# Optimization experiments

Hardware: AMD Instinct MI355X
Metric: run time of the kernel (lower is better)

The kernel has to match this reference:

```python
import jax, jax.numpy as jnp
import numpy as np

B, T, D, NH, FF, L, NCLS, CELL = 4, 64, 128, 4, 512, 2, 7, 64
DIMS = (600, 342, 300)


def layernorm(x, g, b, eps=1e-5):
    m = jnp.mean(x, -1, keepdims=True)
    v = jnp.mean((x - m) ** 2, -1, keepdims=True)
    return (x - m) / jnp.sqrt(v + eps) * g + b


def mha(x, Wqkv, bqkv, Wo, bo):
    N, S, Dm = x.shape
    hd = Dm // NH
    q, k, v = jnp.split(x @ Wqkv + bqkv, 3, axis=-1)
    q = q.reshape(N, S, NH, hd).transpose(0, 2, 1, 3) / jnp.float32(hd) ** 0.5
    k = k.reshape(N, S, NH, hd).transpose(0, 2, 1, 3)
    v = v.reshape(N, S, NH, hd).transpose(0, 2, 1, 3)
    att = jax.nn.softmax(jnp.einsum('nhqd,nhkd->nhqk', q, k), axis=-1)
    o = jnp.einsum('nhqk,nhkd->nhqd', att, v).transpose(0, 2, 1, 3).reshape(N, S, Dm)
    return o @ Wo + bo


def _l2norm(x):
    return x / jnp.maximum(jnp.linalg.norm(x, axis=-1, keepdims=True), 1e-12)


def _model(x_text, x_vis, x_aud, Wp_text, bp_text, Wp_vis, bp_vis, Wp_aud, bp_aud,
           lang1, lang2, Wl1, bl1, Wl2, bl2, phase_text, phase_vis, phase_aud,
           t_Wqkv, t_bqkv, t_Wo, t_bo, t_g1, t_b1, t_W1, t_bf1, t_W2, t_bf2, t_g2, t_b2,
           meas_r, meas_i, fc_W1, fc_b1, fc_W2, fc_b2):
    b, t = x_text.shape[0], x_text.shape[1]
    # modality projections + ReLU
    reps = [jax.nn.relu(x @ W + bb) for x, W, bb in
            ((x_text, Wp_text, bp_text), (x_vis, Wp_vis, bp_vis), (x_aud, Wp_aud, bp_aud))]
    l1 = jnp.broadcast_to(lang1, (b, t, lang1.shape[-1]))
    l2 = jnp.broadcast_to(lang2, (b, t, lang2.shape[-1]))
    lrep1 = jax.nn.relu(l1 @ Wl1 + bl1)
    lrep2 = jax.nn.relu(l2 @ Wl2 + bl2)
    amps = [_l2norm(r) for r in reps]
    lamp1, lamp2 = _l2norm(lrep1), _l2norm(lrep2)
    # phase embedding: smask is all-ones so index is always 0 -> single learned phase vector
    phases = [jnp.broadcast_to(p, (b, t, D)) for p in (phase_text, phase_vis, phase_aud)]
    cmul = lambda ph, a: (a * jnp.cos(ph), a * jnp.sin(ph))
    pure = [cmul(ph, a) for ph, a in zip(phases, amps)]
    ls1 = cmul(phases[0], lamp1)
    ls2 = cmul(phases[0], lamp2)
    # Hadamard gate analog on (real, imag)
    s2 = jnp.float32(2.0) ** -0.5
    h1 = ((ls1[0] + ls1[1]) * s2, (ls1[0] - ls1[1]) * s2)
    h2 = ((ls2[0] + ls2[1]) * s2, (ls2[0] - ls2[1]) * s2)
    # CNOT-style entanglement: complex elementwise product, renormalized to a pure state
    er = h1[0] * h2[0] - h1[1] * h2[1]
    ei = h1[0] * h2[1] + h1[1] * h2[0]
    en = jnp.maximum(jnp.sqrt(jnp.sum(er * er + ei * ei, -1, keepdims=True)), 1e-12)
    ent = (er / en, ei / en)

    def outer(st):  # rho = v v^dagger, v = r + i*im
        r, i = st
        rr = jnp.einsum('btd,bte->btde', r, r) + jnp.einsum('btd,bte->btde', i, i)
        ri = jnp.einsum('btd,bte->btde', i, r) - jnp.einsum('btd,bte->btde', r, i)
        return rr, ri

    mats = [outer(s) for s in pure] + [outer(ent)]
    w = jnp.concatenate([jnp.linalg.norm(r, axis=-1, keepdims=True)
                         for r in reps + [lrep1]], -1)
    w = jax.nn.softmax(w, -1)  # [B,T,4]
    rho_r = sum(w[..., m:m + 1, None] * mats[m][0] for m in range(4))
    rho_i = sum(w[..., m:m + 1, None] * mats[m][1] for m in range(4))
    # seq blocks: same block applied independently per timestep to real and imag parts
    # -> vectorize the Python loop over T (and the real/imag pair) into one batch dim
    x = jnp.concatenate([rho_r, rho_i], 0).reshape(2 * b * t, D, D)
    for l in range(L):
        x = layernorm(x + mha(x, t_Wqkv[l], t_bqkv[l], t_Wo[l], t_bo[l]), t_g1[l], t_b1[l])
        x = layernorm(x + (jax.nn.relu(x @ t_W1[l] + t_bf1[l]) @ t_W2[l] + t_bf2[l]),
                      t_g2[l], t_b2[l])
    x = x.reshape(2, b, t, D, D)
    rho_r, rho_i = x[0], x[1]
    # quantum measurement: p_k = Re(v_k^dagger rho v_k), v_k normalized complex vectors
    mn = jnp.maximum(jnp.sqrt(jnp.sum(meas_r ** 2 + meas_i ** 2, -1, keepdims=True)), 1e-12)
    vr, vi = meas_r / mn, meas_i / mn  # [K=D, D]
    ar = jnp.einsum('btde,ke->btkd', rho_r, vr) - jnp.einsum('btde,ke->btkd', rho_i, vi)
    ai = jnp.einsum('btde,ke->btkd', rho_r, vi) + jnp.einsum('btde,ke->btkd', rho_i, vr)
    probs = jnp.einsum('kd,btkd->btk', vr, ar) + jnp.einsum('kd,btkd->btk', vi, ai)
    logits = jax.nn.relu(probs @ fc_W1 + fc_b1) @ fc_W2 + fc_b2
    return jax.nn.log_softmax(logits, -1)  # [B,T,NCLS]


def setup_inputs():
    key = jax.random.key(0)
    ks = iter(jax.random.split(key, 32))
    rn = lambda shape, s=0.05: jax.random.normal(next(ks), shape, dtype=jnp.float32) * s
    z = lambda shape: jnp.zeros(shape, jnp.float32)
    o = lambda shape: jnp.ones(shape, jnp.float32)
    return dict(
        x_text=rn((B, T, DIMS[0]), 1.0), x_vis=rn((B, T, DIMS[1]), 1.0), x_aud=rn((B, T, DIMS[2]), 1.0),
        Wp_text=rn((DIMS[0], D)), bp_text=z((D,)),
        Wp_vis=rn((DIMS[1], D)), bp_vis=z((D,)),
        Wp_aud=rn((DIMS[2], D)), bp_aud=z((D,)),
        lang1=rn((1, 1, DIMS[2]), 1.0), lang2=rn((1, 1, DIMS[2]), 1.0),
        Wl1=rn((DIMS[2], D)), bl1=z((D,)), Wl2=rn((DIMS[2], D)), bl2=z((D,)),
        phase_text=rn((D,), 1.0), phase_vis=rn((D,), 1.0), phase_aud=rn((D,), 1.0),
        t_Wqkv=rn((L, D, 3 * D)), t_bqkv=z((L, 3 * D)),
        t_Wo=rn((L, D, D)), t_bo=z((L, D)),
        t_g1=o((L, D)), t_b1=z((L, D)),
        t_W1=rn((L, D, FF)), t_bf1=z((L, FF)),
        t_W2=rn((L, FF, D)), t_bf2=z((L, D)),
        t_g2=o((L, D)), t_b2=z((L, D)),
        meas_r=rn((D, D), 1.0), meas_i=rn((D, D), 1.0),
        fc_W1=rn((D, CELL)), fc_b1=z((CELL,)), fc_W2=rn((CELL, NCLS)), fc_b2=z((NCLS,)),
    )


def reference(x_text, x_vis, x_aud, Wp_text, bp_text, Wp_vis, bp_vis, Wp_aud, bp_aud,
              lang1, lang2, Wl1, bl1, Wl2, bl2, phase_text, phase_vis, phase_aud,
              t_Wqkv, t_bqkv, t_Wo, t_bo, t_g1, t_b1, t_W1, t_bf1, t_W2, t_bf2, t_g2, t_b2,
              meas_r, meas_i, fc_W1, fc_b1, fc_W2, fc_b2):
    return _model(x_text, x_vis, x_aud, Wp_text, bp_text, Wp_vis, bp_vis, Wp_aud, bp_aud,
                  lang1, lang2, Wl1, bl1, Wl2, bl2, phase_text, phase_vis, phase_aud,
                  t_Wqkv, t_bqkv, t_Wo, t_bo, t_g1, t_b1, t_W1, t_bf1, t_W2, t_bf2, t_g2, t_b2,
                  meas_r, meas_i, fc_W1, fc_b1, fc_W2, fc_b2)
```

## Files before the change

kernel.cpp:

```cpp
#include <hip/hip_runtime.h>
#include <hip/hip_bf16.h>

typedef __hip_bfloat16 bf16;
typedef short short8 __attribute__((ext_vector_type(8)));
typedef float f32x4 __attribute__((ext_vector_type(4)));
typedef unsigned uint2v __attribute__((ext_vector_type(2)));

__device__ __forceinline__ float b2f(bf16 v){ return __bfloat162float(v); }

__device__ __forceinline__ short f2bs(float f){
  union { __hip_bfloat16 b; short s; } u; u.b = __float2bfloat16(f); return u.s;
}
__device__ __forceinline__ float bs2f(short s){
  union { short s; __hip_bfloat16 b; } u; u.s = s; return __bfloat162float(u.b);
}
__device__ __forceinline__ unsigned pk2(float a, float b){
  return ((unsigned)(unsigned short)f2bs(a)) | (((unsigned)(unsigned short)f2bs(b)) << 16);
}

__device__ __forceinline__ float wred_sum(float v){
  #pragma unroll
  for (int o = 32; o > 0; o >>= 1) v += __shfl_xor(v, o, 64);
  return v;
}

__device__ __forceinline__ void gload_lds16(const void* g, void* l){
  __builtin_amdgcn_global_load_lds((const __attribute__((address_space(1))) unsigned*)g,
                                   (__attribute__((address_space(3))) unsigned*)l, 16, 0, 0);
}

__device__ __forceinline__ unsigned swzA(unsigned a){ return a ^ (((a >> 8) & 7u) << 4); }
__device__ __forceinline__ unsigned swzB(unsigned a){ return a ^ (((a >> 7) & 3u) << 4); }

template<int DIMN>
__device__ void modality(const float* x, const float* W, const float* bia, const float* ph,
                         float* PURE, float* RNORM, int m, int bt, float* xs, float* red)
{
  int tid = threadIdx.x;
  for (int i = tid; i < DIMN; i += 128) xs[i] = x[bt*DIMN + i];
  __syncthreads();
  float a0 = 0.f, a1 = 0.f, a2 = 0.f, a3 = 0.f;
  int k = 0;
  for (; k + 4 <= DIMN; k += 4){
    a0 = fmaf(xs[k],   W[(k  )*128 + tid], a0);
    a1 = fmaf(xs[k+1], W[(k+1)*128 + tid], a1);
    a2 = fmaf(xs[k+2], W[(k+2)*128 + tid], a2);
    a3 = fmaf(xs[k+3], W[(k+3)*128 + tid], a3);
  }
  for (; k < DIMN; k++) a0 = fmaf(xs[k], W[k*128 + tid], a0);
  float acc = bia[tid] + ((a0 + a1) + (a2 + a3));
  float rep = fmaxf(acc, 0.f);
  float s = wred_sum(rep*rep);
  int wid = tid >> 6, lane = tid & 63;
  if (lane == 0) red[wid] = s;
  __syncthreads();
  float nrm = sqrtf(red[0] + red[1]);
  float amp = rep / fmaxf(nrm, 1e-12f);
  float p = ph[tid];
  PURE[bt*768 + m*128 + tid]       = amp * cosf(p);
  PURE[bt*768 + (3+m)*128 + tid]   = amp * sinf(p);
  if (tid == 0) RNORM[bt*4 + m] = nrm;
}

__global__ void prep_kernel(
    const float* __restrict__ Wqkv, const float* __restrict__ Wo,
    const float* __restrict__ W1, const float* __restrict__ W2,
    short* __restrict__ WqkvT, short* __restrict__ WoT,
    short* __restrict__ W1T, short* __restrict__ W2T,
    const float* xt, const float* xv, const float* xa,
    const float* Wpt, const float* bpt, const float* Wpv, const float* bpv,
    const float* Wpa, const float* bpa,
    const float* pht, const float* phv, const float* pha,
    float* PURE, float* RNORM,
    const float* l1, const float* l2,
    const float* Wl1, const float* bl1, const float* Wl2, const float* bl2,
    float* LANGB,
    const float* mr, const float* mi, float* VMEAS, short* VMEASB)
{
  __shared__ float xs[600];
  __shared__ float xs2a[300];
  __shared__ float red[4];
  __shared__ float tile[32][33];
  int b = blockIdx.x, tid = threadIdx.x;

  if (b < 384){
    int l = b / 192, bb = b - l*192;
    const float* in; short* out; int K, N, kt, nt_;
    bool isW2 = false;
    if (bb < 48)      { in = Wqkv; out = WqkvT; K = 128; N = 384; kt = bb & 3;  nt_ = bb >> 2; }
    else if (bb < 64) { int t = bb-48;  in = Wo; out = WoT; K = 128; N = 128; kt = t & 3;  nt_ = t >> 2; }
    else if (bb < 128){ int t = bb-64;  in = W1; out = W1T; K = 128; N = 512; kt = t & 3;  nt_ = t >> 2; }
    else              { int t = bb-128; in = W2; out = W2T; K = 512; N = 128; kt = t & 15; nt_ = t >> 4; isW2 = true; }
    int base = l * K * N;
    int kk0 = kt*32, nn0 = nt_*32;
    int r0 = tid >> 5, c = tid & 31;
    #pragma unroll
    for (int i = 0; i < 8; i++){
      int r = i*4 + r0;
      tile[r][c] = in[base + (kk0 + r)*N + nn0 + c];
    }
    __syncthreads();
    #pragma unroll
    for (int i = 0; i < 8; i++){
      int rr = i*4 + r0;
      float v = tile[c][rr];
      int oi;
      if (!isW2) oi = (nn0 + rr)*K + kk0 + c;
      else       oi = kt*4096 + (nn0 + rr)*32 + c;
      out[base + oi] = f2bs(v);
    }
    return;
  }
  if (b < 1152){
    int idx = b - 384;
    int bt = idx & 255, m = idx >> 8;
    if (m == 0)      modality<600>(xt, Wpt, bpt, pht, PURE, RNORM, 0, bt, xs, red);
    else if (m == 1) modality<342>(xv, Wpv, bpv, phv, PURE, RNORM, 1, bt, xs, red);
    else             modality<300>(xa, Wpa, bpa, pha, PURE, RNORM, 2, bt, xs, red);
    return;
  }
  if (b >= 1153){
    int k = b - 1153;
    float a = mr[k*128 + tid], bb2 = mi[k*128 + tid];
    float ws = wred_sum(a*a + bb2*bb2);
    int wid = tid >> 6, lane = tid & 63;
    if (lane == 0) red[wid] = ws;
    __syncthreads();
    float inv = 1.f / fmaxf(sqrtf(red[0] + red[1]), 1e-12f);
    float vr = a * inv, vi = bb2 * inv;
    int i = k*128 + tid;
    VMEAS[i]          = vr;
    VMEAS[16384 + i]  = vi;
    VMEASB[i]         = f2bs(vr);
    VMEASB[16384 + i] = f2bs(vi);
    VMEASB[32768 + i] = f2bs(-vi);
    return;
  }
  for (int i = tid; i < 300; i += 128){ xs[i] = l1[i]; xs2a[i] = l2[i]; }
  __syncthreads();
  float p10=0,p11=0,p12=0,p13=0, p20=0,p21=0,p22=0,p23=0;
  for (int k = 0; k < 300; k += 4){
    p10 = fmaf(xs[k],    Wl1[(k  )*128+tid], p10);
    p11 = fmaf(xs[k+1],  Wl1[(k+1)*128+tid], p11);
    p12 = fmaf(xs[k+2],  Wl1[(k+2)*128+tid], p12);
    p13 = fmaf(xs[k+3],  Wl1[(k+3)*128+tid], p13);
    p20 = fmaf(xs2a[k],  Wl2[(k  )*128+tid], p20);
    p21 = fmaf(xs2a[k+1],Wl2[(k+1)*128+tid], p21);
    p22 = fmaf(xs2a[k+2],Wl2[(k+2)*128+tid], p22);
    p23 = fmaf(xs2a[k+3],Wl2[(k+3)*128+tid], p23);
  }
  float a1 = bl1[tid] + ((p10+p11)+(p12+p13));
  float a2 = bl2[tid] + ((p20+p21)+(p22+p23));
  a1 = fmaxf(a1, 0.f); a2 = fmaxf(a2, 0.f);
  int wid = tid >> 6, lane = tid & 63;
  float s1 = wred_sum(a1*a1), s2 = wred_sum(a2*a2);
  if (lane == 0){ red[wid] = s1; red[2+wid] = s2; }
  __syncthreads();
  float n1 = sqrtf(red[0] + red[1]);
  float n2 = sqrtf(red[2] + red[3]);
  float lamp1 = a1 / fmaxf(n1, 1e-12f);
  float lamp2 = a2 / fmaxf(n2, 1e-12f);
  float ph = pht[tid];
  float c = cosf(ph), s = sinf(ph);
  const float s2c = 0.70710678118654752f;
  float h1r = (lamp1*c + lamp1*s)*s2c, h1i = (lamp1*c - lamp1*s)*s2c;
  float h2r = (lamp2*c + lamp2*s)*s2c, h2i = (lamp2*c - lamp2*s)*s2c;
  float er = h1r*h2r - h1i*h2i;
  float ei = h1r*h2i + h1i*h2r;
  __syncthreads();
  float se = wred_sum(er*er + ei*ei);
  if (lane == 0) red[wid] = se;
  __syncthreads();
  float en = fmaxf(sqrtf(red[0] + red[1]), 1e-12f);
  LANGB[tid]       = er / en;
  LANGB[128 + tid] = ei / en;
  if (tid == 0) LANGB[256] = n1;
}

__global__ __launch_bounds__(256) void rho_kernel(const float* PURE, const float* RNORM,
                                                  const float* LANGB, short* Xb)
{
  __shared__ float rv[4][128], iv[4][128], wsm[4];
  int bt = blockIdx.x & 255, half = blockIdx.x >> 8;
  int tid = threadIdx.x;
  for (int i = tid; i < 1024; i += 256){
    int d = i & 127;
    if (i < 768){ int m = i >> 7; float v = PURE[bt*768 + i];
                  if (m < 3) rv[m][d] = v; else iv[m-3][d] = v; }
    else if (i < 896) rv[3][d] = LANGB[d];
    else              iv[3][d] = LANGB[128 + d];
  }
  if (tid == 0){
    float n0 = RNORM[bt*4+0], n1 = RNORM[bt*4+1], n2 = RNORM[bt*4+2], n3 = LANGB[256];
    float mx = fmaxf(fmaxf(n0, n1), fmaxf(n2, n3));
    float e0 = __expf(n0-mx), e1 = __expf(n1-mx), e2 = __expf(n2-mx), e3 = __expf(n3-mx);
    float inv = 1.f / (e0+e1+e2+e3);
    wsm[0]=e0*inv; wsm[1]=e1*inv; wsm[2]=e2*inv; wsm[3]=e3*inv;
  }
  __syncthreads();
  float w0 = wsm[0], w1 = wsm[1], w2 = wsm[2], w3 = wsm[3];
  int lo = half*8192, hi = lo + 8192;
  for (int idx = lo + tid; idx < hi; idx += 256){
    int d = idx >> 7, e = idx & 127;
    float rr = 0.f, ri = 0.f;
    {
      float rd=rv[0][d], re=rv[0][e], id=iv[0][d], ie=iv[0][e];
      rr = fmaf(w0, rd*re + id*ie, rr); ri = fmaf(w0, id*re - rd*ie, ri);
    }{
      float rd=rv[1][d], re=rv[1][e], id=iv[1][d], ie=iv[1][e];
      rr = fmaf(w1, rd*re + id*ie, rr); ri = fmaf(w1, id*re - rd*ie, ri);
    }{
      float rd=rv[2][d], re=rv[2][e], id=iv[2][d], ie=iv[2][e];
      rr = fmaf(w2, rd*re + id*ie, rr); ri = fmaf(w2, id*re - rd*ie, ri);
    }{
      float rd=rv[3][d], re=rv[3][e], id=iv[3][d], ie=iv[3][e];
      rr = fmaf(w3, rd*re + id*ie, rr); ri = fmaf(w3, id*re - rd*ie, ri);
    }
    Xb[(size_t)bt*16384 + idx]        = f2bs(rr);
    Xb[(size_t)(256+bt)*16384 + idx]  = f2bs(ri);
  }
}

__global__ __launch_bounds__(256) void attn_kernel(const short* __restrict__ Xb,
    const short* __restrict__ WqkvT, const float* __restrict__ bqkv,
    bf16* __restrict__ ATTO)
{
  __shared__ __align__(16) char lds_raw[43520];
  short* Vt = (short*)(lds_raw);
  short* Qs = (short*)(lds_raw + 8704);
  short* Ks = (short*)(lds_raw + 18944);
  short* Ps = (short*)(lds_raw + 8704);

  const int n = blockIdx.x, h = blockIdx.y;
  const int tid = threadIdx.x;
  const int wid = tid >> 6, lane = tid & 63;
  const int l15 = lane & 15, quad = lane >> 4;
  const int wb = __builtin_amdgcn_readfirstlane(wid);
  const short* xn = Xb + (size_t)n*16384;
  const char* Wbase = (const char*)WqkvT;

  short8 afr[2][4];
  #pragma unroll
  for (int mi = 0; mi < 2; mi++)
    #pragma unroll
    for (int ks = 0; ks < 4; ks++){
      int row = (wid*2 + mi)*16 + l15;
      afr[mi][ks] = *(const short8*)(xn + row*128 + ks*32 + quad*8);
    }
  #pragma unroll
  for (int j = 0; j < 6; j++){
    int seg = wb*6 + j;
    int slab = seg >> 3;
    unsigned off = (unsigned)((seg & 7)*1024);
    unsigned gbase = (unsigned)((slab*128 + h*32)*256);
    gload_lds16(Wbase + gbase + swzA(off + (unsigned)(lane*16)),
                lds_raw + seg*1024);
  }
  __syncthreads();

  f32x4 acc[2][6];
  #pragma unroll
  for (int mi = 0; mi < 2; mi++)
    #pragma unroll
    for (int nt = 0; nt < 6; nt++){
      f32x4 z = {0.f, 0.f, 0.f, 0.f}; acc[mi][nt] = z;
    }

  #pragma unroll
  for (int ks = 0; ks < 4; ks++){
    #pragma unroll
    for (int nt = 0; nt < 6; nt++){
      int slab = nt >> 1;
      int col = (nt & 1)*16 + l15;
      unsigned a = (unsigned)(col*256 + ks*64 + quad*16);
      short8 bfr = *(const short8*)(lds_raw + slab*8192 + swzA(a));
      #pragma unroll
      for (int mi = 0; mi < 2; mi++)
        acc[mi][nt] = __builtin_amdgcn_mfma_f32_16x16x32_bf16(afr[mi][ks], bfr, acc[mi][nt], 0, 0, 0);
    }
  }
  __syncthreads();

  #pragma unroll
  for (int nt = 0; nt < 6; nt++){
    int sec = nt >> 1;
    int cl = (nt & 1)*16 + l15;
    float bias = bqkv[sec*128 + h*32 + cl];
    #pragma unroll
    for (int mi = 0; mi < 2; mi++){
      int rowb = (wid*2 + mi)*16 + quad*4;
      #pragma unroll
      for (int r = 0; r < 4; r++){
        float v = acc[mi][nt][r] + bias;
        int row = rowb + r;
        if (sec == 0)      Qs[row*40 + cl] = f2bs(v * 0.17677669529663687f);
        else if (sec == 1) Ks[row*40 + cl] = f2bs(v);
        else               Vt[cl*136 + row] = f2bs(v);
      }
    }
  }
  __syncthreads();

  f32x4 s2[8][2];
  {
    short8 qf[2];
    #pragma unroll
    for (int qt = 0; qt < 2; qt++){
      int row = (wid*2 + qt)*16 + l15;
      qf[qt] = *(const short8*)(Qs + row*40 + quad*8);
    }
    #pragma unroll
    for (int kt = 0; kt < 8; kt++){
      int kr = kt*16 + l15;
      short8 kf = *(const short8*)(Ks + kr*40 + quad*8);
      #pragma unroll
      for (int qt = 0; qt < 2; qt++){
        f32x4 z = {0.f, 0.f, 0.f, 0.f};
        s2[kt][qt] = __builtin_amdgcn_mfma_f32_16x16x32_bf16(kf, qf[qt], z, 0, 0, 0);
      }
    }
  }

  #pragma unroll
  for (int qt = 0; qt < 2; qt++){
    float mx = -1e30f;
    #pragma unroll
    for (int kt = 0; kt < 8; kt++)
      #pragma unroll
      for (int r = 0; r < 4; r++) mx = fmaxf(mx, s2[kt][qt][r]);
    mx = fmaxf(mx, __shfl_xor(mx, 16, 64));
    mx = fmaxf(mx, __shfl_xor(mx, 32, 64));
    float sum = 0.f;
    #pragma unroll
    for (int kt = 0; kt < 8; kt++)
      #pragma unroll
      for (int r = 0; r < 4; r++){
        float p = __expf(s2[kt][qt][r] - mx);
        s2[kt][qt][r] = p; sum += p;
      }
    sum += __shfl_xor(sum, 16, 64);
    sum += __shfl_xor(sum, 32, 64);
    float inv = 1.f / sum;
    #pragma unroll
    for (int kt = 0; kt < 8; kt++)
      #pragma unroll
      for (int r = 0; r < 4; r++) s2[kt][qt][r] *= inv;
  }
  __syncthreads();

  #pragma unroll
  for (int kt = 0; kt < 8; kt++){
    #pragma unroll
    for (int qt = 0; qt < 2; qt++){
      int q  = (wid*2 + qt)*16 + l15;
      int k0 = kt*16 + quad*4;
      uint2v v;
      v.x = pk2(s2[kt][qt][0], s2[kt][qt][1]);
      v.y = pk2(s2[kt][qt][2], s2[kt][qt][3]);
      *(uint2v*)((char*)Ps + (unsigned)(q*272 + k0*2)) = v;
    }
  }
  __syncthreads();

  f32x4 o_[2][2];
  #pragma unroll
  for (int mi = 0; mi < 2; mi++)
    #pragma unroll
    for (int n2 = 0; n2 < 2; n2++){
      f32x4 z = {0.f, 0.f, 0.f, 0.f}; o_[mi][n2] = z;
    }
  #pragma unroll
  for (int ks = 0; ks < 4; ks++){
    short8 pf[2];
    #pragma unroll
    for (int mi = 0; mi < 2; mi++){
      int row = (wid*2 + mi)*16 + l15;
      pf[mi] = *(const short8*)(Ps + row*136 + ks*32 + quad*8);
    }
    #pragma unroll
    for (int n2 = 0; n2 < 2; n2++){
      short8 vf = *(const short8*)(Vt + (n2*16 + l15)*136 + ks*32 + quad*8);
      #pragma unroll
      for (int mi = 0; mi < 2; mi++)
        o_[mi][n2] = __builtin_amdgcn_mfma_f32_16x16x32_bf16(pf[mi], vf, o_[mi][n2], 0, 0, 0);
    }
  }
  bf16* on = ATTO + (size_t)n*16384;
  #pragma unroll
  for (int mi = 0; mi < 2; mi++){
    int rowb = (wid*2 + mi)*16 + quad*4;
    #pragma unroll
    for (int n2 = 0; n2 < 2; n2++){
      int col = h*32 + n2*16 + l15;
      #pragma unroll
      for (int r = 0; r < 4; r++)
        on[(rowb + r)*128 + col] = __float2bfloat16(o_[mi][n2][r]);
    }
  }
}

__global__ __launch_bounds__(256, 2) void proj_ffn_kernel(const bf16* __restrict__ SRC,
    short* __restrict__ Xb, const short* __restrict__ WoT,
    const float* __restrict__ bo, const float* __restrict__ g1v,
    const float* __restrict__ bb1,
    const short* __restrict__ W1T, const float* __restrict__ bf1,
    const short* __restrict__ W2C, const float* __restrict__ bf2,
    const float* __restrict__ g2v, const float* __restrict__ bb2)
{
  __shared__ __align__(16) char lds_raw[65536];
  __shared__ float bf1L[512];
  const int n = blockIdx.x, tid = threadIdx.x;
  const int wid = tid >> 6, lane = tid & 63;
  const int l15 = lane & 15, quad = lane >> 4;
  const int wb = __builtin_amdgcn_readfirstlane(wid);
  const short* an = (const short*)SRC + (size_t)n*16384;
  short* xn = Xb + (size_t)n*16384;
  char* XsB = lds_raw + 32768;
  short* Hs = (short*)(lds_raw + 32768);

  short8 af[2][4];
  #pragma unroll
  for (int mi = 0; mi < 2; mi++)
    #pragma unroll
    for (int ks = 0; ks < 4; ks++){
      int row = wid*32 + mi*16 + l15;
      af[mi][ks] = *(const short8*)(an + row*128 + ks*32 + quad*8);
    }
  #pragma unroll
  for (int j = 0; j < 8; j++){
    unsigned L = (unsigned)(j*4096 + wb*1024 + lane*16);
    gload_lds16((const char*)WoT + swzA(L), lds_raw + (j*4096 + wb*1024));
    gload_lds16((const char*)xn  + swzA(L), XsB + (j*4096 + wb*1024));
  }
  for (int i = tid; i < 512; i += 256) bf1L[i] = bf1[i];
  float bov[8], g1a[8], b1a[8];
  #pragma unroll
  for (int nt = 0; nt < 8; nt++){
    int col = nt*16 + l15;
    bov[nt] = bo[col]; g1a[nt] = g1v[col]; b1a[nt] = bb1[col];
  }
  __syncthreads();

  f32x4 Y[2][8];
  #pragma unroll
  for (int mi = 0; mi < 2; mi++)
    #pragma unroll
    for (int nt = 0; nt < 8; nt++){ f32x4 z = {0.f,0.f,0.f,0.f}; Y[mi][nt] = z; }
  #pragma unroll
  for (int ks = 0; ks < 4; ks++){
    #pragma unroll
    for (int nt = 0; nt < 8; nt++){
      unsigned a = (unsigned)((nt*16 + l15)*256 + ks*64 + quad*16);
      short8 bh = *(const short8*)(lds_raw + swzA(a));
      #pragma unroll
      for (int mi = 0; mi < 2; mi++)
        Y[mi][nt] = __builtin_amdgcn_mfma_f32_16x16x32_bf16(af[mi][ks], bh, Y[mi][nt], 0, 0, 0);
    }
  }
  __syncthreads();

  #pragma unroll
  for (int j = 0; j < 2; j++){
    unsigned L = (unsigned)(j*4096 + wb*1024 + lane*16);
    gload_lds16((const char*)W1T + swzA(L), lds_raw + (j*4096 + wb*1024));
    gload_lds16((const char*)W2C + swzB(L), lds_raw + (8192 + j*4096 + wb*1024));
  }

  unsigned yv1p[2][4][4];
  #pragma unroll
  for (int mi = 0; mi < 2; mi++){
    #pragma unroll
    for (int r = 0; r < 4; r++){
      int row = wid*32 + mi*16 + quad*4 + r;
      float yv[8]; float S = 0.f, Q = 0.f;
      #pragma unroll
      for (int nt = 0; nt < 8; nt++){
        int col = nt*16 + l15;
        float res = bs2f(*(const short*)(XsB + swzA((unsigned)(row*256 + col*2))));
        float y = Y[mi][nt][r] + bov[nt] + res;
        yv[nt] = y; S += y; Q += y*y;
      }
      #pragma unroll
      for (int o = 1; o < 16; o <<= 1){ S += __shfl_xor(S, o, 64); Q += __shfl_xor(Q, o, 64); }
      float m = S * (1.f/128.f);
      float var = Q * (1.f/128.f) - m*m;
      float inv = rsqrtf(var + 1e-5f);
      #pragma unroll
      for (int nt = 0; nt < 8; nt++){
        int col = nt*16 + l15;
        short ob = f2bs((yv[nt] - m) * inv * g1a[nt] + b1a[nt]);
        *(short*)(XsB + swzA((unsigned)(row*256 + col*2))) = ob;
        unsigned u = (unsigned)(unsigned short)ob;
        if ((nt & 1) == 0) yv1p[mi][r][nt>>1] = u;
        else               yv1p[mi][r][nt>>1] |= (u << 16);
      }
    }
  }

  short8 af2[2][4];
  #pragma unroll
  for (int mi = 0; mi < 2; mi++)
    #pragma unroll
    for (int ks = 0; ks < 4; ks++){
      int row = wid*32 + mi*16 + l15;
      unsigned a = (unsigned)(row*256 + ks*64 + quad*16);
      af2[mi][ks] = *(const short8*)(XsB + swzA(a));
    }
  __syncthreads();

  f32x4 Y2[2][8];
  #pragma unroll
  for (int mi = 0; mi < 2; mi++)
    #pragma unroll
    for (int nt = 0; nt < 8; nt++){ f32x4 z = {0.f,0.f,0.f,0.f}; Y2[mi][nt] = z; }

  for (int c = 0; c < 16; c++){
    const int cb = c & 1;
    if (c < 15){
      const int nb = cb ^ 1;
      #pragma unroll
      for (int j = 0; j < 2; j++){
        unsigned L = (unsigned)(j*4096 + wb*1024 + lane*16);
        gload_lds16((const char*)W1T + (unsigned)((c+1)*8192) + swzA(L),
                    lds_raw + (nb*16384 + j*4096 + wb*1024));
        gload_lds16((const char*)W2C + (unsigned)((c+1)*8192) + swzB(L),
                    lds_raw + (nb*16384 + 8192 + j*4096 + wb*1024));
      }
      asm volatile("s_waitcnt vmcnt(4)" ::: "memory");
    } else {
      asm volatile("s_waitcnt vmcnt(0)" ::: "memory");
    }
    __builtin_amdgcn_sched_barrier(0);
    __builtin_amdgcn_s_barrier();
    __builtin_amdgcn_sched_barrier(0);

    const char* bW1 = lds_raw + cb*16384;
    const char* bW2 = lds_raw + cb*16384 + 8192;

    f32x4 Hc[2][2];
    #pragma unroll
    for (int mi = 0; mi < 2; mi++)
      #pragma unroll
      for (int nt2 = 0; nt2 < 2; nt2++){ f32x4 z = {0.f,0.f,0.f,0.f}; Hc[mi][nt2] = z; }
    #pragma unroll
    for (int ks = 0; ks < 4; ks++){
      #pragma unroll
      for (int nt2 = 0; nt2 < 2; nt2++){
        unsigned a = (unsigned)((nt2*16 + l15)*256 + ks*64 + quad*16);
        short8 bh = *(const short8*)(bW1 + swzA(a));
        #pragma unroll
        for (int mi = 0; mi < 2; mi++)
          Hc[mi][nt2] = __builtin_amdgcn_mfma_f32_16x16x32_bf16(af2[mi][ks], bh, Hc[mi][nt2], 0, 0, 0);
      }
    }
    float b1v0 = bf1L[c*32 + l15];
    float b1v1 = bf1L[c*32 + 16 + l15];
    #pragma unroll
    for (int nt2 = 0; nt2 < 2; nt2++){
      int col = nt2*16 + l15;
      float b1v = nt2 ? b1v1 : b1v0;
      #pragma unroll
      for (int mi = 0; mi < 2; mi++){
        int rowb = wid*32 + mi*16 + quad*4;
        #pragma unroll
        for (int r = 0; r < 4; r++)
          Hs[(rowb + r)*40 + col] = f2bs(fmaxf(Hc[mi][nt2][r] + b1v, 0.f));
      }
    }
    short8 ph[2];
    #pragma unroll
    for (int mi = 0; mi < 2; mi++){
      int row = wid*32 + mi*16 + l15;
      ph[mi] = *(const short8*)(Hs + row*40 + quad*8);
    }
    #pragma unroll
    for (int nt = 0; nt < 8; nt++){
      unsigned a = (unsigned)((nt*16 + l15)*64 + quad*16);
      short8 bh = *(const short8*)(bW2 + swzB(a));
      #pragma unroll
      for (int mi = 0; mi < 2; mi++)
        Y2[mi][nt] = __builtin_amdgcn_mfma_f32_16x16x32_bf16(ph[mi], bh, Y2[mi][nt], 0, 0, 0);
    }
    __builtin_amdgcn_sched_barrier(0);
    __builtin_amdgcn_s_barrier();
    __builtin_amdgcn_sched_barrier(0);
  }

  {
    float b2v[8], gv[8], bbv[8];
    #pragma unroll
    for (int nt = 0; nt < 8; nt++){
      int col = nt*16 + l15;
      b2v[nt] = bf2[col]; gv[nt] = g2v[col]; bbv[nt] = bb2[col];
    }
    #pragma unroll
    for (int mi = 0; mi < 2; mi++){
      #pragma unroll
      for (int r = 0; r < 4; r++){
        int row = wid*32 + mi*16 + quad*4 + r;
        float yv[8]; float S = 0.f, Q = 0.f;
        #pragma unroll
        for (int nt = 0; nt < 8; nt++){
          unsigned u = yv1p[mi][r][nt>>1];
          short rs = (short)((nt & 1) ? (u >> 16) : (u & 0xffffu));
          float y = Y2[mi][nt][r] + b2v[nt] + bs2f(rs);
          yv[nt] = y; S += y; Q += y*y;
        }
        #pragma unroll
        for (int o = 1; o < 16; o <<= 1){ S += __shfl_xor(S, o, 64); Q += __shfl_xor(Q, o, 64); }
        float m = S * (1.f/128.f);
        float var = Q * (1.f/128.f) - m*m;
        float inv = rsqrtf(var + 1e-5f);
        #pragma unroll
        for (int nt = 0; nt < 8; nt++){
          int col = nt*16 + l15;
          xn[row*128 + col] = f2bs((yv[nt] - m) * inv * gv[nt] + bbv[nt]);
        }
      }
    }
  }
}

__global__ __launch_bounds__(512) void probs_head_kernel(const short* __restrict__ Xb,
    const float* __restrict__ VMEAS, const short* __restrict__ VMEASB,
    const float* __restrict__ W1, const float* __restrict__ b1,
    const float* __restrict__ W2, const float* __restrict__ b2,
    float* __restrict__ out)
{
  __shared__ __align__(16) char lds_raw[24576];
  __shared__ float sp[128];
  __shared__ float hsh[64];
  __shared__ float lg[7];
  __shared__ float mred[2];
  const int bt = blockIdx.x, tid = threadIdx.x;
  const int wid = tid >> 6, lane = tid & 63;
  const int l15 = lane & 15, quad = lane >> 4;
  const int wb = __builtin_amdgcn_readfirstlane(wid);
  const int zh = wb >> 2;
  const int zq = wb & 3;
  const short* R = Xb + (size_t)bt*16384;
  const short* I = Xb + (size_t)(256+bt)*16384;

  if (tid < 128) sp[tid] = 0.f;

  const int drow = zh*64 + zq*16 + l15;
  short8 aR[4], aI[4];
  #pragma unroll
  for (int ks = 0; ks < 4; ks++){
    aR[ks] = *(const short8*)(R + drow*128 + ks*32 + quad*8);
    aI[ks] = *(const short8*)(I + drow*128 + ks*32 + quad*8);
  }

  #define STAGE_NT(nt_, buf_)                                                  \
    { _Pragma("unroll")                                                        \
      for (int j = 0; j < 2; j++){                                             \
        int seg = wb*2 + j;                              \
        if (seg < 12){                                                         \
          int s = seg >> 2;                                     \
          unsigned off = (unsigned)((seg & 3)*1024);                           \
          gload_lds16((const char*)VMEASB + s*32768 + (nt_)*4096 +             \
                        swzA(off + (unsigned)(lane*16)),                       \
                      lds_raw + (buf_)*12288 + s*4096 + (int)off);             \
        }                                                                      \
      } }

  STAGE_NT(0, 0)
  __syncthreads();

  const int db0 = zh*64 + zq*16 + quad*4;

  for (int nt = 0; nt < 8; nt++){
    const int cb = nt & 1;
    int k = nt*16 + l15;
    f32x4 vR = *(const f32x4*)(VMEAS + k*128 + db0);
    f32x4 vI = *(const f32x4*)(VMEAS + 16384 + k*128 + db0);
    if (nt < 7){
      STAGE_NT(nt+1, cb^1)
      asm volatile("s_waitcnt vmcnt(2)" ::: "memory");
    } else {
      asm volatile("s_waitcnt vmcnt(0)" ::: "memory");
    }
    __builtin_amdgcn_sched_barrier(0);
    __builtin_amdgcn_s_barrier();
    __builtin_amdgcn_sched_barrier(0);

    const char* bvr = lds_raw + cb*12288;
    const char* bvi = bvr + 4096;
    const char* bnv = bvr + 8192;

    f32x4 Ar = {0.f,0.f,0.f,0.f}, Ai = {0.f,0.f,0.f,0.f};
    #pragma unroll
    for (int ks = 0; ks < 4; ks++){
      unsigned a = swzA((unsigned)(l15*256 + ks*64 + quad*16));
      short8 b_vr = *(const short8*)(bvr + a);
      short8 b_vi = *(const short8*)(bvi + a);
      short8 b_nv = *(const short8*)(bnv + a);
      Ar = __builtin_amdgcn_mfma_f32_16x16x32_bf16(aR[ks], b_vr, Ar, 0, 0, 0);
      Ar = __builtin_amdgcn_mfma_f32_16x16x32_bf16(aI[ks], b_nv, Ar, 0, 0, 0);
      Ai = __builtin_amdgcn_mfma_f32_16x16x32_bf16(aR[ks], b_vi, Ai, 0, 0, 0);
      Ai = __builtin_amdgcn_mfma_f32_16x16x32_bf16(aI[ks], b_vr, Ai, 0, 0, 0);
    }

    float pv = 0.f;
    #pragma unroll
    for (int r = 0; r < 4; r++) pv += vR[r]*Ar[r] + vI[r]*Ai[r];
    pv += __shfl_xor(pv, 16, 64);
    pv += __shfl_xor(pv, 32, 64);
    if (quad == 0) atomicAdd(&sp[nt*16 + l15], pv);

    __builtin_amdgcn_sched_barrier(0);
    __builtin_amdgcn_s_barrier();
    __builtin_amdgcn_sched_barrier(0);
  }
  #undef STAGE_NT

  __syncthreads();
  if (tid < 64){
    float a0 = b1[tid], a1 = 0.f, a2 = 0.f, a3 = 0.f;
    for (int d = 0; d < 128; d += 4){
      a0 = fmaf(sp[d  ], W1[(d  )*64 + tid], a0);
      a1 = fmaf(sp[d+1], W1[(d+1)*64 + tid], a1);
      a2 = fmaf(sp[d+2], W1[(d+2)*64 + tid], a2);
      a3 = fmaf(sp[d+3], W1[(d+3)*64 + tid], a3);
    }
    hsh[tid] = fmaxf((a0 + a1) + (a2 + a3), 0.f);
  }
  __syncthreads();
  if (tid < 7){
    float a = b2[tid];
    for (int j = 0; j < 64; j++) a = fmaf(hsh[j], W2[j*7 + tid], a);
    lg[tid] = a;
  }
  __syncthreads();
  if (tid == 0){
    float M = -1e30f;
    for (int c = 0; c < 7; c++) M = fmaxf(M, lg[c]);
    float S = 0.f;
    for (int c = 0; c < 7; c++) S += __expf(lg[c] - M);
    mred[0] = M; mred[1] = logf(S);
  }
  __syncthreads();
  if (tid < 7) out[bt*7 + tid] = lg[tid] - mred[0] - mred[1];
}

extern "C" void kernel_launch(void* const* d_in, const int* in_sizes, int n_in,
                              void* d_out, int out_size, void* d_ws, size_t ws_size,
                              hipStream_t stream)
{
  (void)in_sizes; (void)n_in; (void)out_size; (void)ws_size;
  const float* xt   = (const float*)d_in[0];
  const float* xv   = (const float*)d_in[1];
  const float* xa   = (const float*)d_in[2];
  const float* Wpt  = (const float*)d_in[3];
  const float* bpt  = (const float*)d_in[4];
  const float* Wpv  = (const float*)d_in[5];
  const float* bpv  = (const float*)d_in[6];
  const float* Wpa  = (const float*)d_in[7];
  const float* bpa  = (const float*)d_in[8];
  const float* l1   = (const float*)d_in[9];
  const float* l2   = (const float*)d_in[10];
  const float* Wl1  = (const float*)d_in[11];
  const float* bl1  = (const float*)d_in[12];
  const float* Wl2  = (const float*)d_in[13];
  const float* bl2  = (const float*)d_in[14];
  const float* pht  = (const float*)d_in[15];
  const float* phv  = (const float*)d_in[16];
  const float* pha  = (const float*)d_in[17];
  const float* Wqkv = (const float*)d_in[18];
  const float* bqkv = (const float*)d_in[19];
  const float* Wo   = (const float*)d_in[20];
  const float* bo   = (const float*)d_in[21];
  const float* g1   = (const float*)d_in[22];
  const float* b1   = (const float*)d_in[23];
  const float* W1   = (const float*)d_in[24];
  const float* bf1  = (const float*)d_in[25];
  const float* W2   = (const float*)d_in[26];
  const float* bf2  = (const float*)d_in[27];
  const float* g2   = (const float*)d_in[28];
  const float* b2   = (const float*)d_in[29];
  const float* mr   = (const float*)d_in[30];
  const float* mi   = (const float*)d_in[31];
  const float* fcW1 = (const float*)d_in[32];
  const float* fcb1 = (const float*)d_in[33];
  const float* fcW2 = (const float*)d_in[34];
  const float* fcb2 = (const float*)d_in[35];
  float* out = (float*)d_out;

  char* wsb = (char*)d_ws;
  short* Xb     = (short*)(wsb);
  bf16*  ATTO   = (bf16*) (wsb + 16777216);
  float* PURE   = (float*)(wsb + 33554432);
  float* RNORM  = (float*)(wsb + 34340864);
  float* LANGB  = (float*)(wsb + 34344960);
  float* VMEAS  = (float*)(wsb + 34347008);
  short* WqkvT  = (short*)(wsb + 34740224);
  short* WoT    = (short*)(wsb + 34936832);
  short* W1T    = (short*)(wsb + 35002368);
  short* W2T    = (short*)(wsb + 35264512);
  short* VMEASB = (short*)(wsb + 35526656);

  prep_kernel<<<1281, 128, 0, stream>>>(Wqkv, Wo, W1, W2, WqkvT, WoT, W1T, W2T,
                                        xt, xv, xa, Wpt, bpt, Wpv, bpv, Wpa, bpa,
                                        pht, phv, pha, PURE, RNORM,
                                        l1, l2, Wl1, bl1, Wl2, bl2, LANGB,
                                        mr, mi, VMEAS, VMEASB);

  rho_kernel<<<512, 256, 0, stream>>>(PURE, RNORM, LANGB, Xb);

  for (int l = 0; l < 2; l++){
    attn_kernel<<<dim3(512, 4), 256, 0, stream>>>(Xb, WqkvT + (size_t)l*49152,
                                                  bqkv + (size_t)l*384, ATTO);
    proj_ffn_kernel<<<512, 256, 0, stream>>>(ATTO, Xb,
                                             WoT + (size_t)l*16384,
                                             bo + (size_t)l*128, g1 + (size_t)l*128,
                                             b1 + (size_t)l*128,
                                             W1T + (size_t)l*65536, bf1 + (size_t)l*512,
                                             W2T + (size_t)l*65536, bf2 + (size_t)l*128,
                                             g2 + (size_t)l*128, b2 + (size_t)l*128);
  }

  probs_head_kernel<<<256, 512, 0, stream>>>(Xb, VMEAS, VMEASB,
                                             fcW1, fcb1, fcW2, fcb2, out);
}
```

Before: 279.0 us.

## Use 8 waves per block in attention and FFN kernels, one 16-row tile each

```diff
diff --git a/kernel.cpp b/kernel.cpp
--- a/kernel.cpp
+++ b/kernel.cpp
@@ -221,7 +221,7 @@
   }
 }
 
-__global__ __launch_bounds__(256) void attn_kernel(const short* __restrict__ Xb,
+__global__ __launch_bounds__(512, 4) void attn_kernel(const short* __restrict__ Xb,
     const short* __restrict__ WqkvT, const float* __restrict__ bqkv,
     bf16* __restrict__ ATTO)
 {
@@ -239,17 +239,15 @@
   const short* xn = Xb + (size_t)n*16384;
   const char* Wbase = (const char*)WqkvT;
 
-  short8 afr[2][4];
-  #pragma unroll
-  for (int mi = 0; mi < 2; mi++)
-    #pragma unroll
-    for (int ks = 0; ks < 4; ks++){
-      int row = (wid*2 + mi)*16 + l15;
-      afr[mi][ks] = *(const short8*)(xn + row*128 + ks*32 + quad*8);
-    }
-  #pragma unroll
-  for (int j = 0; j < 6; j++){
-    int seg = wb*6 + j;
+  short8 afr[4];
+  #pragma unroll
+  for (int ks = 0; ks < 4; ks++){
+    int row = wid*16 + l15;
+    afr[ks] = *(const short8*)(xn + row*128 + ks*32 + quad*8);
+  }
+  #pragma unroll
+  for (int j = 0; j < 3; j++){
+    int seg = wb*3 + j;
     int slab = seg >> 3;
     unsigned off = (unsigned)((seg & 7)*1024);
     unsigned gbase = (unsigned)((slab*128 + h*32)*256);
@@ -258,13 +256,9 @@
   }
   __syncthreads();
 
-  f32x4 acc[2][6];
-  #pragma unroll
-  for (int mi = 0; mi < 2; mi++)
-    #pragma unroll
-    for (int nt = 0; nt < 6; nt++){
-      f32x4 z = {0.f, 0.f, 0.f, 0.f}; acc[mi][nt] = z;
-    }
+  f32x4 acc[6];
+  #pragma unroll
+  for (int nt = 0; nt < 6; nt++){ f32x4 z = {0.f,0.f,0.f,0.f}; acc[nt] = z; }
 
   #pragma unroll
   for (int ks = 0; ks < 4; ks++){
@@ -274,9 +268,7 @@
       int col = (nt & 1)*16 + l15;
       unsigned a = (unsigned)(col*256 + ks*64 + quad*16);
       short8 bfr = *(const short8*)(lds_raw + slab*8192 + swzA(a));
-      #pragma unroll
-      for (int mi = 0; mi < 2; mi++)
-        acc[mi][nt] = __builtin_amdgcn_mfma_f32_16x16x32_bf16(afr[mi][ks], bfr, acc[mi][nt], 0, 0, 0);
+      acc[nt] = __builtin_amdgcn_mfma_f32_16x16x32_bf16(afr[ks], bfr, acc[nt], 0, 0, 0);
     }
   }
   __syncthreads();
@@ -286,48 +278,35 @@
     int sec = nt >> 1;
     int cl = (nt & 1)*16 + l15;
     float bias = bqkv[sec*128 + h*32 + cl];
-    #pragma unroll
-    for (int mi = 0; mi < 2; mi++){
-      int rowb = (wid*2 + mi)*16 + quad*4;
-      #pragma unroll
-      for (int r = 0; r < 4; r++){
-        float v = acc[mi][nt][r] + bias;
-        int row = rowb + r;
-        if (sec == 0)      Qs[row*40 + cl] = f2bs(v * 0.17677669529663687f);
-        else if (sec == 1) Ks[row*40 + cl] = f2bs(v);
-        else               Vt[cl*136 + row] = f2bs(v);
-      }
-    }
-  }
-  __syncthreads();
-
-  f32x4 s2[8][2];
+    int rowb = wid*16 + quad*4;
+    #pragma unroll
+    for (int r = 0; r < 4; r++){
+      float v = acc[nt][r] + bias;
+      int row = rowb + r;
+      if (sec == 0)      Qs[row*40 + cl] = f2bs(v * 0.17677669529663687f);
+      else if (sec == 1) Ks[row*40 + cl] = f2bs(v);
+      else               Vt[cl*136 + row] = f2bs(v);
+    }
+  }
+  __syncthreads();
+
+  f32x4 s2[8];
   {
-    short8 qf[2];
-    #pragma unroll
-    for (int qt = 0; qt < 2; qt++){
-      int row = (wid*2 + qt)*16 + l15;
-      qf[qt] = *(const short8*)(Qs + row*40 + quad*8);
-    }
+    short8 qf = *(const short8*)(Qs + (wid*16 + l15)*40 + quad*8);
     #pragma unroll
     for (int kt = 0; kt < 8; kt++){
-      int kr = kt*16 + l15;
-      short8 kf = *(const short8*)(Ks + kr*40 + quad*8);
-      #pragma unroll
-      for (int qt = 0; qt < 2; qt++){
-        f32x4 z = {0.f, 0.f, 0.f, 0.f};
-        s2[kt][qt] = __builtin_amdgcn_mfma_f32_16x16x32_bf16(kf, qf[qt], z, 0, 0, 0);
-      }
-    }
-  }
-
-  #pragma unroll
-  for (int qt = 0; qt < 2; qt++){
+      short8 kf = *(const short8*)(Ks + (kt*16 + l15)*40 + quad*8);
+      f32x4 z = {0.f, 0.f, 0.f, 0.f};
+      s2[kt] = __builtin_amdgcn_mfma_f32_16x16x32_bf16(kf, qf, z, 0, 0, 0);
+    }
+  }
+
+  {
     float mx = -1e30f;
     #pragma unroll
     for (int kt = 0; kt < 8; kt++)
       #pragma unroll
-      for (int r = 0; r < 4; r++) mx = fmaxf(mx, s2[kt][qt][r]);
+      for (int r = 0; r < 4; r++) mx = fmaxf(mx, s2[kt][r]);
     mx = fmaxf(mx, __shfl_xor(mx, 16, 64));
     mx = fmaxf(mx, __shfl_xor(mx, 32, 64));
     float sum = 0.f;
@@ -335,8 +314,8 @@
     for (int kt = 0; kt < 8; kt++)
       #pragma unroll
       for (int r = 0; r < 4; r++){
-        float p = __expf(s2[kt][qt][r] - mx);
-        s2[kt][qt][r] = p; sum += p;
+        float p = __expf(s2[kt][r] - mx);
+        s2[kt][r] = p; sum += p;
       }
     sum += __shfl_xor(sum, 16, 64);
     sum += __shfl_xor(sum, 32, 64);
@@ -344,62 +323,49 @@
     #pragma unroll
     for (int kt = 0; kt < 8; kt++)
       #pragma unroll
-      for (int r = 0; r < 4; r++) s2[kt][qt][r] *= inv;
-  }
-  __syncthreads();
-
-  #pragma unroll
-  for (int kt = 0; kt < 8; kt++){
-    #pragma unroll
-    for (int qt = 0; qt < 2; qt++){
-      int q  = (wid*2 + qt)*16 + l15;
+      for (int r = 0; r < 4; r++) s2[kt][r] *= inv;
+  }
+  __syncthreads();
+
+  {
+    int q = wid*16 + l15;
+    #pragma unroll
+    for (int kt = 0; kt < 8; kt++){
       int k0 = kt*16 + quad*4;
       uint2v v;
-      v.x = pk2(s2[kt][qt][0], s2[kt][qt][1]);
-      v.y = pk2(s2[kt][qt][2], s2[kt][qt][3]);
+      v.x = pk2(s2[kt][0], s2[kt][1]);
+      v.y = pk2(s2[kt][2], s2[kt][3]);
       *(uint2v*)((char*)Ps + (unsigned)(q*272 + k0*2)) = v;
     }
   }
   __syncthreads();
 
-  f32x4 o_[2][2];
-  #pragma unroll
-  for (int mi = 0; mi < 2; mi++)
-    #pragma unroll
-    for (int n2 = 0; n2 < 2; n2++){
-      f32x4 z = {0.f, 0.f, 0.f, 0.f}; o_[mi][n2] = z;
-    }
+  f32x4 o_[2];
+  #pragma unroll
+  for (int n2 = 0; n2 < 2; n2++){ f32x4 z = {0.f,0.f,0.f,0.f}; o_[n2] = z; }
   #pragma unroll
   for (int ks = 0; ks < 4; ks++){
-    short8 pf[2];
-    #pragma unroll
-    for (int mi = 0; mi < 2; mi++){
-      int row = (wid*2 + mi)*16 + l15;
-      pf[mi] = *(const short8*)(Ps + row*136 + ks*32 + quad*8);
-    }
+    short8 pf = *(const short8*)(Ps + (wid*16 + l15)*136 + ks*32 + quad*8);
     #pragma unroll
     for (int n2 = 0; n2 < 2; n2++){
       short8 vf = *(const short8*)(Vt + (n2*16 + l15)*136 + ks*32 + quad*8);
-      #pragma unroll
-      for (int mi = 0; mi < 2; mi++)
-        o_[mi][n2] = __builtin_amdgcn_mfma_f32_16x16x32_bf16(pf[mi], vf, o_[mi][n2], 0, 0, 0);
+      o_[n2] = __builtin_amdgcn_mfma_f32_16x16x32_bf16(pf, vf, o_[n2], 0, 0, 0);
     }
   }
   bf16* on = ATTO + (size_t)n*16384;
-  #pragma unroll
-  for (int mi = 0; mi < 2; mi++){
-    int rowb = (wid*2 + mi)*16 + quad*4;
+  {
+    int rowb = wid*16 + quad*4;
     #pragma unroll
     for (int n2 = 0; n2 < 2; n2++){
       int col = h*32 + n2*16 + l15;
       #pragma unroll
       for (int r = 0; r < 4; r++)
-        on[(rowb + r)*128 + col] = __float2bfloat16(o_[mi][n2][r]);
-    }
-  }
-}
-
-__global__ __launch_bounds__(256, 2) void proj_ffn_kernel(const bf16* __restrict__ SRC,
+        on[(rowb + r)*128 + col] = __float2bfloat16(o_[n2][r]);
+    }
+  }
+}
+
+__global__ __launch_bounds__(512, 4) void proj_ffn_kernel(const bf16* __restrict__ SRC,
     short* __restrict__ Xb, const short* __restrict__ WoT,
     const float* __restrict__ bo, const float* __restrict__ g1v,
     const float* __restrict__ bb1,
@@ -418,21 +384,20 @@
   char* XsB = lds_raw + 32768;
   short* Hs = (short*)(lds_raw + 32768);
 
-  short8 af[2][4];
-  #pragma unroll
-  for (int mi = 0; mi < 2; mi++)
-    #pragma unroll
-    for (int ks = 0; ks < 4; ks++){
-      int row = wid*32 + mi*16 + l15;
-      af[mi][ks] = *(const short8*)(an + row*128 + ks*32 + quad*8);
-    }
-  #pragma unroll
-  for (int j = 0; j < 8; j++){
-    unsigned L = (unsigned)(j*4096 + wb*1024 + lane*16);
-    gload_lds16((const char*)WoT + swzA(L), lds_raw + (j*4096 + wb*1024));
-    gload_lds16((const char*)xn  + swzA(L), XsB + (j*4096 + wb*1024));
-  }
-  for (int i = tid; i < 512; i += 256) bf1L[i] = bf1[i];
+  short8 af[4];
+  #pragma unroll
+  for (int ks = 0; ks < 4; ks++){
+    int row = wid*16 + l15;
+    af[ks] = *(const short8*)(an + row*128 + ks*32 + quad*8);
+  }
+  #pragma unroll
+  for (int j = 0; j < 4; j++){
+    int seg = wb*4 + j;
+    unsigned L = (unsigned)(seg*1024 + lane*16);
+    gload_lds16((const char*)WoT + swzA(L), lds_raw + seg*1024);
+    gload_lds16((const char*)xn  + swzA(L), XsB + seg*1024);
+  }
+  for (int i = tid; i < 512; i += 512) bf1L[i] = bf1[i];
   float bov[8], g1a[8], b1a[8];
   #pragma unroll
   for (int nt = 0; nt < 8; nt++){
@@ -441,43 +406,138 @@
   }
   __syncthreads();
 
-  f32x4 Y[2][8];
-  #pragma unroll
-  for (int mi = 0; mi < 2; mi++)
-    #pragma unroll
-    for (int nt = 0; nt < 8; nt++){ f32x4 z = {0.f,0.f,0.f,0.f}; Y[mi][nt] = z; }
+  f32x4 Y[8];
+  #pragma unroll
+  for (int nt = 0; nt < 8; nt++){ f32x4 z = {0.f,0.f,0.f,0.f}; Y[nt] = z; }
   #pragma unroll
   for (int ks = 0; ks < 4; ks++){
     #pragma unroll
     for (int nt = 0; nt < 8; nt++){
       unsigned a = (unsigned)((nt*16 + l15)*256 + ks*64 + quad*16);
       short8 bh = *(const short8*)(lds_raw + swzA(a));
-      #pragma unroll
-      for (int mi = 0; mi < 2; mi++)
-        Y[mi][nt] = __builtin_amdgcn_mfma_f32_16x16x32_bf16(af[mi][ks], bh, Y[mi][nt], 0, 0, 0);
-    }
-  }
-  __syncthreads();
-
-  #pragma unroll
-  for (int j = 0; j < 2; j++){
-    unsigned L = (unsigned)(j*4096 + wb*1024 + lane*16);
-    gload_lds16((const char*)W1T + swzA(L), lds_raw + (j*4096 + wb*1024));
-    gload_lds16((const char*)W2C + swzB(L), lds_raw + (8192 + j*4096 + wb*1024));
-  }
-
-  unsigned yv1p[2][4][4];
-  #pragma unroll
-  for (int mi = 0; mi < 2; mi++){
+      Y[nt] = __builtin_amdgcn_mfma_f32_16x16x32_bf16(af[ks], bh, Y[nt], 0, 0, 0);
+    }
+  }
+  __syncthreads();
+
+  {
+    unsigned L = (unsigned)(wb*1024 + lane*16);
+    gload_lds16((const char*)W1T + swzA(L), lds_raw + wb*1024);
+    gload_lds16((const char*)W2C + swzB(L), lds_raw + 8192 + wb*1024);
+  }
+
+  unsigned yv1p[4][4];
+  #pragma unroll
+  for (int r = 0; r < 4; r++){
+    int row = wid*16 + quad*4 + r;
+    float yv[8]; float S = 0.f, Q = 0.f;
+    #pragma unroll
+    for (int nt = 0; nt < 8; nt++){
+      int col = nt*16 + l15;
+      float res = bs2f(*(const short*)(XsB + swzA((unsigned)(row*256 + col*2))));
+      float y = Y[nt][r] + bov[nt] + res;
+      yv[nt] = y; S += y; Q += y*y;
+    }
+    #pragma unroll
+    for (int o = 1; o < 16; o <<= 1){ S += __shfl_xor(S, o, 64); Q += __shfl_xor(Q, o, 64); }
+    float m = S * (1.f/128.f);
+    float var = Q * (1.f/128.f) - m*m;
+    float inv = rsqrtf(var + 1e-5f);
+    #pragma unroll
+    for (int nt = 0; nt < 8; nt++){
+      int col = nt*16 + l15;
+      short ob = f2bs((yv[nt] - m) * inv * g1a[nt] + b1a[nt]);
+      *(short*)(XsB + swzA((unsigned)(row*256 + col*2))) = ob;
+      unsigned u = (unsigned)(unsigned short)ob;
+      if ((nt & 1) == 0) yv1p[r][nt>>1] = u;
+      else               yv1p[r][nt>>1] |= (u << 16);
+    }
+  }
+
+  short8 af2[4];
+  #pragma unroll
+  for (int ks = 0; ks < 4; ks++){
+    int row = wid*16 + l15;
+    unsigned a = (unsigned)(row*256 + ks*64 + quad*16);
+    af2[ks] = *(const short8*)(XsB + swzA(a));
+  }
+  __syncthreads();
+
+  f32x4 Y2[8];
+  #pragma unroll
+  for (int nt = 0; nt < 8; nt++){ f32x4 z = {0.f,0.f,0.f,0.f}; Y2[nt] = z; }
+
+  for (int c = 0; c < 16; c++){
+    const int cb = c & 1;
+    if (c < 15){
+      const int nb = cb ^ 1;
+      unsigned L = (unsigned)(wb*1024 + lane*16);
+      gload_lds16((const char*)W1T + (unsigned)((c+1)*8192) + swzA(L),
+                  lds_raw + (nb*16384 + wb*1024));
+      gload_lds16((const char*)W2C + (unsigned)((c+1)*8192) + swzB(L),
+                  lds_raw + (nb*16384 + 8192 + wb*1024));
+      asm volatile("s_waitcnt vmcnt(2)" ::: "memory");
+    } else {
+      asm volatile("s_waitcnt vmcnt(0)" ::: "memory");
+    }
+    __builtin_amdgcn_sched_barrier(0);
+    __builtin_amdgcn_s_barrier();
+    __builtin_amdgcn_sched_barrier(0);
+
+    const char* bW1 = lds_raw + cb*16384;
+    const char* bW2 = lds_raw + cb*16384 + 8192;
+
+    f32x4 Hc[2];
+    #pragma unroll
+    for (int nt2 = 0; nt2 < 2; nt2++){ f32x4 z = {0.f,0.f,0.f,0.f}; Hc[nt2] = z; }
+    #pragma unroll
+    for (int ks = 0; ks < 4; ks++){
+      #pragma unroll
+      for (int nt2 = 0; nt2 < 2; nt2++){
+        unsigned a = (unsigned)((nt2*16 + l15)*256 + ks*64 + quad*16);
+        short8 bh = *(const short8*)(bW1 + swzA(a));
+        Hc[nt2] = __builtin_amdgcn_mfma_f32_16x16x32_bf16(af2[ks], bh, Hc[nt2], 0, 0, 0);
+      }
+    }
+    float b1v0 = bf1L[c*32 + l15];
+    float b1v1 = bf1L[c*32 + 16 + l15];
+    #pragma unroll
+    for (int nt2 = 0; nt2 < 2; nt2++){
+      int col = nt2*16 + l15;
+      float b1v = nt2 ? b1v1 : b1v0;
+      int rowb = wid*16 + quad*4;
+      #pragma unroll
+      for (int r = 0; r < 4; r++)
+        Hs[(rowb + r)*40 + col] = f2bs(fmaxf(Hc[nt2][r] + b1v, 0.f));
+    }
+    short8 ph = *(const short8*)(Hs + (wid*16 + l15)*40 + quad*8);
+    #pragma unroll
+    for (int nt = 0; nt < 8; nt++){
+      unsigned a = (unsigned)((nt*16 + l15)*64 + quad*16);
+      short8 bh = *(const short8*)(bW2 + swzB(a));
+      Y2[nt] = __builtin_amdgcn_mfma_f32_16x16x32_bf16(ph, bh, Y2[nt], 0, 0, 0);
+    }
+    __builtin_amdgcn_sched_barrier(0);
+    __builtin_amdgcn_s_barrier();
+    __builtin_amdgcn_sched_barrier(0);
+  }
+
+  {
+    float b2v[8], gv[8], bbv[8];
+    #pragma unroll
+    for (int nt = 0; nt < 8; nt++){
+      int col = nt*16 + l15;
+      b2v[nt] = bf2[col]; gv[nt] = g2v[col]; bbv[nt] = bb2[col];
+    }
     #pragma unroll
     for (int r = 0; r < 4; r++){
-      int row = wid*32 + mi*16 + quad*4 + r;
+      int row = wid*16 + quad*4 + r;
       float yv[8]; float S = 0.f, Q = 0.f;
       #pragma unroll
       for (int nt = 0; nt < 8; nt++){
-        int col = nt*16 + l15;
-        float res = bs2f(*(const short*)(XsB + swzA((unsigned)(row*256 + col*2))));
-        float y = Y[mi][nt][r] + bov[nt] + res;
+        unsigned u = yv1p[r][nt>>1];
+        short rs = (short)((nt & 1) ? (u >> 16) : (u & 0xffffu));
+        float y = Y2[nt][r] + b2v[nt] + bs2f(rs);
         yv[nt] = y; S += y; Q += y*y;
       }
       #pragma unroll
@@ -488,134 +548,7 @@
       #pragma unroll
       for (int nt = 0; nt < 8; nt++){
         int col = nt*16 + l15;
-        short ob = f2bs((yv[nt] - m) * inv * g1a[nt] + b1a[nt]);
-        *(short*)(XsB + swzA((unsigned)(row*256 + col*2))) = ob;
-        unsigned u = (unsigned)(unsigned short)ob;
-        if ((nt & 1) == 0) yv1p[mi][r][nt>>1] = u;
-        else               yv1p[mi][r][nt>>1] |= (u << 16);
-      }
-    }
-  }
-
-  short8 af2[2][4];
-  #pragma unroll
-  for (int mi = 0; mi < 2; mi++)
-    #pragma unroll
-    for (int ks = 0; ks < 4; ks++){
-      int row = wid*32 + mi*16 + l15;
-      unsigned a = (unsigned)(row*256 + ks*64 + quad*16);
-      af2[mi][ks] = *(const short8*)(XsB + swzA(a));
-    }
-  __syncthreads();
-
-  f32x4 Y2[2][8];
-  #pragma unroll
-  for (int mi = 0; mi < 2; mi++)
-    #pragma unroll
-    for (int nt = 0; nt < 8; nt++){ f32x4 z = {0.f,0.f,0.f,0.f}; Y2[mi][nt] = z; }
-
-  for (int c = 0; c < 16; c++){
-    const int cb = c & 1;
-    if (c < 15){
-      const int nb = cb ^ 1;
-      #pragma unroll
-      for (int j = 0; j < 2; j++){
-        unsigned L = (unsigned)(j*4096 + wb*1024 + lane*16);
-        gload_lds16((const char*)W1T + (unsigned)((c+1)*8192) + swzA(L),
-                    lds_raw + (nb*16384 + j*4096 + wb*1024));
-        gload_lds16((const char*)W2C + (unsigned)((c+1)*8192) + swzB(L),
-                    lds_raw + (nb*16384 + 8192 + j*4096 + wb*1024));
-      }
-      asm volatile("s_waitcnt vmcnt(4)" ::: "memory");
-    } else {
-      asm volatile("s_waitcnt vmcnt(0)" ::: "memory");
-    }
-    __builtin_amdgcn_sched_barrier(0);
-    __builtin_amdgcn_s_barrier();
-    __builtin_amdgcn_sched_barrier(0);
-
-    const char* bW1 = lds_raw + cb*16384;
-    const char* bW2 = lds_raw + cb*16384 + 8192;
-
-    f32x4 Hc[2][2];
-    #pragma unroll
-    for (int mi = 0; mi < 2; mi++)
-      #pragma unroll
-      for (int nt2 = 0; nt2 < 2; nt2++){ f32x4 z = {0.f,0.f,0.f,0.f}; Hc[mi][nt2] = z; }
-    #pragma unroll
-    for (int ks = 0; ks < 4; ks++){
-      #pragma unroll
-      for (int nt2 = 0; nt2 < 2; nt2++){
-        unsigned a = (unsigned)((nt2*16 + l15)*256 + ks*64 + quad*16);
-        short8 bh = *(const short8*)(bW1 + swzA(a));
-        #pragma unroll
-        for (int mi = 0; mi < 2; mi++)
-          Hc[mi][nt2] = __builtin_amdgcn_mfma_f32_16x16x32_bf16(af2[mi][ks], bh, Hc[mi][nt2], 0, 0, 0);
-      }
-    }
-    float b1v0 = bf1L[c*32 + l15];
-    float b1v1 = bf1L[c*32 + 16 + l15];
-    #pragma unroll
-    for (int nt2 = 0; nt2 < 2; nt2++){
-      int col = nt2*16 + l15;
-      float b1v = nt2 ? b1v1 : b1v0;
-      #pragma unroll
-      for (int mi = 0; mi < 2; mi++){
-        int rowb = wid*32 + mi*16 + quad*4;
-        #pragma unroll
-        for (int r = 0; r < 4; r++)
-          Hs[(rowb + r)*40 + col] = f2bs(fmaxf(Hc[mi][nt2][r] + b1v, 0.f));
-      }
-    }
-    short8 ph[2];
-    #pragma unroll
-    for (int mi = 0; mi < 2; mi++){
-      int row = wid*32 + mi*16 + l15;
-      ph[mi] = *(const short8*)(Hs + row*40 + quad*8);
-    }
-    #pragma unroll
-    for (int nt = 0; nt < 8; nt++){
-      unsigned a = (unsigned)((nt*16 + l15)*64 + quad*16);
-      short8 bh = *(const short8*)(bW2 + swzB(a));
-      #pragma unroll
-      for (int mi = 0; mi < 2; mi++)
-        Y2[mi][nt] = __builtin_amdgcn_mfma_f32_16x16x32_bf16(ph[mi], bh, Y2[mi][nt], 0, 0, 0);
-    }
-    __builtin_amdgcn_sched_barrier(0);
-    __builtin_amdgcn_s_barrier();
-    __builtin_amdgcn_sched_barrier(0);
-  }
-
-  {
-    float b2v[8], gv[8], bbv[8];
-    #pragma unroll
-    for (int nt = 0; nt < 8; nt++){
-      int col = nt*16 + l15;
-      b2v[nt] = bf2[col]; gv[nt] = g2v[col]; bbv[nt] = bb2[col];
-    }
-    #pragma unroll
-    for (int mi = 0; mi < 2; mi++){
-      #pragma unroll
-      for (int r = 0; r < 4; r++){
-        int row = wid*32 + mi*16 + quad*4 + r;
-        float yv[8]; float S = 0.f, Q = 0.f;
-        #pragma unroll
-        for (int nt = 0; nt < 8; nt++){
-          unsigned u = yv1p[mi][r][nt>>1];
-          short rs = (short)((nt & 1) ? (u >> 16) : (u & 0xffffu));
-          float y = Y2[mi][nt][r] + b2v[nt] + bs2f(rs);
-          yv[nt] = y; S += y; Q += y*y;
-        }
-        #pragma unroll
-        for (int o = 1; o < 16; o <<= 1){ S += __shfl_xor(S, o, 64); Q += __shfl_xor(Q, o, 64); }
-        float m = S * (1.f/128.f);
-        float var = Q * (1.f/128.f) - m*m;
-        float inv = rsqrtf(var + 1e-5f);
-        #pragma unroll
-        for (int nt = 0; nt < 8; nt++){
-          int col = nt*16 + l15;
-          xn[row*128 + col] = f2bs((yv[nt] - m) * inv * gv[nt] + bbv[nt]);
-        }
+        xn[row*128 + col] = f2bs((yv[nt] - m) * inv * gv[nt] + bbv[nt]);
       }
     }
   }
@@ -808,9 +741,9 @@
   rho_kernel<<<512, 256, 0, stream>>>(PURE, RNORM, LANGB, Xb);
 
   for (int l = 0; l < 2; l++){
-    attn_kernel<<<dim3(512, 4), 256, 0, stream>>>(Xb, WqkvT + (size_t)l*49152,
+    attn_kernel<<<dim3(512, 4), 512, 0, stream>>>(Xb, WqkvT + (size_t)l*49152,
                                                   bqkv + (size_t)l*384, ATTO);
-    proj_ffn_kernel<<<512, 256, 0, stream>>>(ATTO, Xb,
+    proj_ffn_kernel<<<512, 512, 0, stream>>>(ATTO, Xb,
                                              WoT + (size_t)l*16384,
                                              bo + (size_t)l*128, g1 + (size_t)l*128,
                                              b1 + (size_t)l*128,
```

Result: no change. 281.2 us (+0.8%).
